# Optimization experiments

Measured on AMD Instinct MI355X. Metric: run time of the kernel, lower is better.

## Reference

```python
import jax, jax.numpy as jnp
import numpy as np

EPS = 1e-5
DIM_HEAD = 64
HEADS = 8

def layernorm(x, gamma, beta):
    mu = jnp.mean(x, axis=-1, keepdims=True)
    var = jnp.var(x, axis=-1, keepdims=True)
    return (x - mu) * jax.lax.rsqrt(var + EPS) * gamma + beta

def setup_inputs() -> dict:
    key = jax.random.key(0)
    ks = jax.random.split(key, 8)
    b, n, dh = 1, 896, 3072       # batch, enformer seq len, enformer_hidden_dim
    c, j, dc = 64, 127, 1024      # num contexts (tracks), context len, context_dim
    inner = HEADS * DIM_HEAD      # 512
    return {
        "embeddings": jax.random.normal(ks[0], (b, n, dh), jnp.float32),
        "context": jax.random.normal(ks[1], (c, j, dc), jnp.float32),
        "context_mask": jax.random.randint(ks[2], (b, j), 0, 2) > 0,
        "q_gamma": jnp.ones((dh,), jnp.float32),
        "q_beta": jnp.zeros((dh,), jnp.float32),
        "kv_gamma": jnp.ones((dc,), jnp.float32),
        "kv_beta": jnp.zeros((dc,), jnp.float32),
        "Wq": jax.random.normal(ks[3], (dh, inner), jnp.float32) * 0.02,
        "Wkv": jax.random.normal(ks[4], (dc, 2 * inner), jnp.float32) * 0.02,
        "null_k": jax.random.normal(ks[5], (inner,), jnp.float32),
        "null_v": jax.random.normal(ks[6], (inner,), jnp.float32),
        "Wo": jax.random.normal(ks[7], (inner, dh), jnp.float32) * 0.02,
        "bo": jnp.zeros((dh,), jnp.float32),
        "Wp": jax.random.normal(jax.random.fold_in(key, 9), (dh, 1), jnp.float32) * 0.02,
        "bp": jnp.zeros((1,), jnp.float32),
    }

def reference(embeddings, context, context_mask, q_gamma, q_beta, kv_gamma, kv_beta,
              Wq, Wkv, null_k, null_v, Wo, bo, Wp, bp):
    h, d = HEADS, DIM_HEAD
    scale = d ** -0.5
    b, n, dh = embeddings.shape
    c = context.shape[0]
    # projections
    q = layernorm(embeddings, q_gamma, q_beta) @ Wq            # (b, n, h*d)
    kv = layernorm(context, kv_gamma, kv_beta) @ Wkv           # (c, j, 2*h*d)
    k, v = jnp.split(kv, 2, axis=-1)
    # prepend null key/value token
    k = jnp.concatenate([jnp.broadcast_to(null_k, (c, 1, h * d)), k], axis=1)
    v = jnp.concatenate([jnp.broadcast_to(null_v, (c, 1, h * d)), v], axis=1)
    # split heads: (b, h, i, d) / (c, h, j, d)
    q = q.reshape(b, n, h, d).transpose(0, 2, 1, 3)
    k = k.reshape(c, -1, h, d).transpose(0, 2, 1, 3)
    v = v.reshape(c, -1, h, d).transpose(0, 2, 1, 3)
    sim = jnp.einsum('bhid,chjd->bchij', q, k) * scale         # (b, c, h, i, j+1)
    # mask: pad with True for the null token, broadcast over c, h, i
    mask = jnp.pad(context_mask, ((0, 0), (1, 0)), constant_values=True)
    sim = jnp.where(mask[:, None, None, None, :], sim, -jnp.finfo(sim.dtype).max)
    attn = jax.nn.softmax(sim, axis=-1)
    out = jnp.einsum('bchij,chjd->bchid', attn, v)             # (b, c, h, i, d)
    out = out.transpose(0, 1, 3, 2, 4).reshape(b, c, n, h * d)  # (b, c, n, h*d)
    branch = out @ Wo + bo                                     # (b, c, n, dh)
    emb = embeddings[:, None] + branch                         # (b, c, n, dh)
    pred = jax.nn.softplus((emb @ Wp + bp)[..., 0])            # (b, c, n)
    return pred.transpose(0, 2, 1)                             # (b, n, c)
```

## Files before the change

kernel.cpp:

```cpp
#include <hip/hip_runtime.h>
#include <math.h>

#define N_SEQ   896
#define DH      3072
#define NCTX    64
#define JLEN    127
#define DC      1024
#define HEADS   8
#define DHEAD   64
#define INNER   512
#define MKV     8128
#define MKVPAD  8192

typedef __bf16 bf16x8 __attribute__((ext_vector_type(8)));
typedef float  f32x4  __attribute__((ext_vector_type(4)));

#define OFF_EDOT   0LL
#define OFF_QBF    (OFF_EDOT + N_SEQ)
#define OFF_KBF    (OFF_QBF  + (long long)N_SEQ*INNER/2)
#define OFF_VPM    (OFF_KBF  + (long long)NCTX*128*INNER/2)
#define OFF_VPNULL (OFF_VPM  + (long long)MKV*8)
#define OFF_WOP    (OFF_VPNULL + 8)
#define OFF_BOP    (OFF_WOP  + INNER)
#define OFF_SBUF   (OFF_BOP  + 16)
#define OFF_ANQ    (OFF_SBUF + (long long)NCTX*HEADS*N_SEQ)
#define OFF_ANKV   (OFF_ANQ  + (long long)N_SEQ*DH/2)
#define OFF_WQT    (OFF_ANKV + (long long)MKVPAD*DC/2)
#define OFF_WKT    (OFF_WQT  + (long long)INNER*DH/2)
#define OFF_WVPT   (OFF_WKT  + (long long)INNER*DC/2)
#define OFF_QSL    (OFF_WVPT + 16*1024/2)

__device__ __forceinline__ void async_copy16(const __bf16* g, __bf16* l) {
    __builtin_amdgcn_global_load_lds(
        (const __attribute__((address_space(1))) unsigned int*)g,
        (__attribute__((address_space(3))) unsigned int*)l,
        16, 0, 0);
}

#define B_Q0   10
#define B_T0   (B_Q0 + 224)
#define B_KV0  (B_T0 + 2048)
#define GRID1  (B_KV0 + 2032)

__global__ __launch_bounds__(256)
void prep_all_kernel(const float* __restrict__ emb, const float* __restrict__ ctx,
                     const float* __restrict__ qg, const float* __restrict__ qb_,
                     const float* __restrict__ kvg, const float* __restrict__ kvb,
                     const float* __restrict__ Wq, const float* __restrict__ Wkv,
                     const float* __restrict__ Wo, const float* __restrict__ bo,
                     const float* __restrict__ Wp,
                     const float* __restrict__ nullk, const float* __restrict__ nullv,
                     __bf16* __restrict__ ANQ, __bf16* __restrict__ ANKV,
                     __bf16* __restrict__ WQT, __bf16* __restrict__ WKT,
                     __bf16* __restrict__ WVPT, float* __restrict__ VPNULL,
                     float* __restrict__ EDOT, float* __restrict__ BOP,
                     __bf16* __restrict__ KBF)
{
    __shared__ float tT[32][33];
    const int bid = blockIdx.x, tid = threadIdx.x;
    const int lane = tid & 63, wid = tid >> 6;

    if (bid < 8) {
        int h = bid;
        float* wops = &tT[0][0];
        int d = tid >> 2, part = tid & 3;
        const float* worow = Wo + (long long)(h * 64 + d) * DH;
        float s = 0.f;
        #pragma unroll 8
        for (int k = part * 4; k < DH; k += 16) {
            float4 a = *(const float4*)&worow[k];
            float4 w = *(const float4*)&Wp[k];
            s += a.x*w.x + a.y*w.y + a.z*w.z + a.w*w.w;
        }
        s += __shfl_xor(s, 1); s += __shfl_xor(s, 2);
        if (part == 0) wops[d] = s;
        __syncthreads();
        if (tid < 64) {
            float v = nullv[h * 64 + tid] * wops[tid];
            #pragma unroll
            for (int o = 1; o < 64; o <<= 1) v += __shfl_xor(v, o);
            if (tid == 0) VPNULL[h] = v;
        }
        #pragma unroll
        for (int kk = 0; kk < 4; ++kk) {
            int k = tid + kk * 256;
            const float* src = Wkv + (long long)k * (2 * INNER) + INNER + h * 64;
            float s2 = 0.f;
            #pragma unroll
            for (int d2 = 0; d2 < 64; d2 += 4) {
                float4 a = *(const float4*)&src[d2];
                s2 += a.x*wops[d2] + a.y*wops[d2+1] + a.z*wops[d2+2] + a.w*wops[d2+3];
            }
            WVPT[h * 1024 + k] = (__bf16)s2;
        }
    } else if (bid == 8) {
        float* red = &tT[0][0];
        float s = 0.f;
        #pragma unroll
        for (int i = 0; i < 3; ++i) {
            int k = i * 1024 + tid * 4;
            float4 a = *(const float4*)&bo[k];
            float4 w = *(const float4*)&Wp[k];
            s += a.x*w.x + a.y*w.y + a.z*w.z + a.w*w.w;
        }
        #pragma unroll
        for (int o = 1; o < 64; o <<= 1) s += __shfl_xor(s, o);
        if (lane == 0) red[wid] = s;
        __syncthreads();
        if (tid == 0) *BOP = red[0] + red[1] + red[2] + red[3];
    } else if (bid == 9) {
        for (int i = tid; i < 8 * 1024; i += 256)
            WVPT[8 * 1024 + i] = (__bf16)0.f;
        for (int i = tid; i < NCTX * INNER; i += 256) {
            int c = i >> 9, d2 = i & 511;
            KBF[(long long)(c * 128) * INNER + d2] = (__bf16)nullk[d2];
        }
    } else if (bid < B_T0) {
        int r = (bid - B_Q0) * 4 + wid;
        const float* x = emb + (long long)r * DH;
        float s = 0.f, ss = 0.f, dp = 0.f;
        #pragma unroll
        for (int c = 0; c < 12; ++c) {
            int col = c * 256 + lane * 4;
            float4 a = *(const float4*)&x[col];
            float4 w = *(const float4*)&Wp[col];
            s  += a.x + a.y + a.z + a.w;
            ss += a.x*a.x + a.y*a.y + a.z*a.z + a.w*a.w;
            dp += a.x*w.x + a.y*w.y + a.z*w.z + a.w*w.w;
        }
        #pragma unroll
        for (int o = 1; o < 64; o <<= 1) {
            s += __shfl_xor(s, o); ss += __shfl_xor(ss, o); dp += __shfl_xor(dp, o);
        }
        float m  = s * (1.f / DH);
        float rs = rsqrtf(ss * (1.f / DH) - m * m + 1e-5f);
        __bf16* op = ANQ + (long long)r * DH;
        #pragma unroll
        for (int c = 0; c < 12; ++c) {
            int col = c * 256 + lane * 4;
            float4 a  = *(const float4*)&x[col];
            float4 g4 = *(const float4*)&qg[col];
            float4 b4 = *(const float4*)&qb_[col];
            __bf16 ov[4];
            ov[0] = (__bf16)((a.x - m) * rs * g4.x + b4.x);
            ov[1] = (__bf16)((a.y - m) * rs * g4.y + b4.y);
            ov[2] = (__bf16)((a.z - m) * rs * g4.z + b4.z);
            ov[3] = (__bf16)((a.w - m) * rs * g4.w + b4.w);
            *(ushort4*)&op[col] = *(ushort4*)ov;
        }
        if (lane == 0) EDOT[r] = dp;
    } else if (bid < B_KV0) {
        int t = bid - B_T0;
        const float* src; __bf16* dst; int srcS, dstS, rb, cb;
        if (t < 1536) {
            rb = (t >> 4) * 32; cb = (t & 15) * 32;
            src = Wq; srcS = INNER; dst = WQT; dstS = DH;
        } else {
            int bi = t - 1536;
            rb = (bi >> 4) * 32; cb = (bi & 15) * 32;
            src = Wkv; srcS = 2 * INNER; dst = WKT; dstS = DC;
        }
        int tx = tid & 31, ty = tid >> 5;
        #pragma unroll
        for (int i = 0; i < 32; i += 8)
            tT[ty + i][tx] = src[(long long)(rb + ty + i) * srcS + cb + tx];
        __syncthreads();
        #pragma unroll
        for (int i = 0; i < 32; i += 8)
            dst[(long long)(cb + ty + i) * dstS + rb + tx] = (__bf16)tT[tx][ty + i];
    } else {
        int r = (bid - B_KV0) * 4 + wid;
        const float* x = ctx + (long long)r * DC;
        float4 xv[4];
        float s = 0.f, ss = 0.f;
        #pragma unroll
        for (int c = 0; c < 4; ++c) {
            xv[c] = *(const float4*)&x[c * 256 + lane * 4];
            s  += xv[c].x + xv[c].y + xv[c].z + xv[c].w;
            ss += xv[c].x*xv[c].x + xv[c].y*xv[c].y + xv[c].z*xv[c].z + xv[c].w*xv[c].w;
        }
        #pragma unroll
        for (int o = 1; o < 64; o <<= 1) { s += __shfl_xor(s, o); ss += __shfl_xor(ss, o); }
        float m  = s * (1.f / DC);
        float rs = rsqrtf(ss * (1.f / DC) - m * m + 1e-5f);
        __bf16* op = ANKV + (long long)r * DC;
        #pragma unroll
        for (int c = 0; c < 4; ++c) {
            int col = c * 256 + lane * 4;
            float4 g4 = *(const float4*)&kvg[col];
            float4 b4 = *(const float4*)&kvb[col];
            __bf16 ov[4];
            ov[0] = (__bf16)((xv[c].x - m) * rs * g4.x + b4.x);
            ov[1] = (__bf16)((xv[c].y - m) * rs * g4.y + b4.y);
            ov[2] = (__bf16)((xv[c].z - m) * rs * g4.z + b4.z);
            ov[3] = (__bf16)((xv[c].w - m) * rs * g4.w + b4.w);
            *(ushort4*)&op[col] = *(ushort4*)ov;
        }
    }
}

__global__ __launch_bounds__(256)
void proj_kernel(const __bf16* __restrict__ ANQ, const __bf16* __restrict__ WQT,
                 const __bf16* __restrict__ ANKV, const __bf16* __restrict__ WKT,
                 const __bf16* __restrict__ WVPT,
                 __bf16* __restrict__ qbf, __bf16* __restrict__ kout,
                 float* __restrict__ vpm) {
    __shared__ __align__(16) __bf16 As[128 * 32];
    __shared__ __align__(16) __bf16 Bs[128 * 32];
    int b = blockIdx.x;
    int tid = threadIdx.x;
    int lane = tid & 63, w = tid >> 6;
    int n16 = lane & 15, quad = lane >> 4;
    int wr = (w >> 1) * 64, wc = (w & 1) * 64;

    const __bf16 *A, *B;
    int K, kend, mode;
    long long m0, n0;
    if (b < 28) {
        mode = 0;
        m0 = (long long)(b % 7) * 128;
        n0 = (long long)(b / 7) * 128;
        K = DH; kend = DH;
        A = ANQ; B = WQT;
    } else {
        mode = 1;
        int b2 = b - 28;
        m0 = (long long)(b2 & 63) * 128;
        n0 = (long long)(b2 >> 6) * 128;
        K = DC; kend = DC;
        A = ANKV; B = WKT;
    }
    bool dovp = (mode == 1) && (n0 == 0);

    const __bf16* aG = A + (m0 + (tid >> 2)) * K + (tid & 3) * 8;
    const __bf16* bG = B + (n0 + (tid >> 2)) * K + (tid & 3) * 8;
    __bf16* aL = As + tid * 8;
    __bf16* bL = Bs + tid * 8;

    f32x4 acc[4][4], accv[4];
    const f32x4 z = {0.f, 0.f, 0.f, 0.f};
    #pragma unroll
    for (int i = 0; i < 4; ++i) {
        accv[i] = z;
        #pragma unroll
        for (int j = 0; j < 4; ++j) acc[i][j] = z;
    }

    for (int k0 = 0; k0 < kend; k0 += 32) {
        async_copy16(aG + k0, aL);
        async_copy16(aG + (long long)64 * K + k0, aL + 2048);
        async_copy16(bG + k0, bL);
        async_copy16(bG + (long long)64 * K + k0, bL + 2048);
        bf16x8 bv;
        if (dovp) bv = *(const bf16x8*)&WVPT[n16 * 1024 + k0 + quad * 8];
        __syncthreads();
        bf16x8 af[4], bfr[4];
        #pragma unroll
        for (int i = 0; i < 4; ++i)
            af[i]  = *(const bf16x8*)&As[(wr + i * 16 + n16) * 32 + quad * 8];
        #pragma unroll
        for (int j = 0; j < 4; ++j)
            bfr[j] = *(const bf16x8*)&Bs[(wc + j * 16 + n16) * 32 + quad * 8];
        #pragma unroll
        for (int i = 0; i < 4; ++i)
            #pragma unroll
            for (int j = 0; j < 4; ++j)
                acc[i][j] = __builtin_amdgcn_mfma_f32_16x16x32_bf16(af[i], bfr[j], acc[i][j], 0, 0, 0);
        if (dovp) {
            #pragma unroll
            for (int i = 0; i < 4; ++i)
                accv[i] = __builtin_amdgcn_mfma_f32_16x16x32_bf16(af[i], bv, accv[i], 0, 0, 0);
        }
        __syncthreads();
    }

    if (mode == 0) {
        #pragma unroll
        for (int i = 0; i < 4; ++i)
            #pragma unroll
            for (int r = 0; r < 4; ++r) {
                long long gr = m0 + wr + i * 16 + quad * 4 + r;
                #pragma unroll
                for (int j = 0; j < 4; ++j) {
                    long long gc = n0 + wc + j * 16 + n16;
                    qbf[gr * INNER + gc] = (__bf16)acc[i][j][r];
                }
            }
    } else {
        #pragma unroll
        for (int i = 0; i < 4; ++i)
            #pragma unroll
            for (int r = 0; r < 4; ++r) {
                long long gr = m0 + wr + i * 16 + quad * 4 + r;
                if (gr >= MKV) continue;
                int cc = (int)(gr / JLEN), jj = (int)(gr % JLEN);
                #pragma unroll
                for (int j = 0; j < 4; ++j) {
                    long long gc = n0 + wc + j * 16 + n16;
                    kout[((long long)(cc * 128) + jj + 1) * INNER + gc] = (__bf16)acc[i][j][r];
                }
                if (dovp && n16 < 8) vpm[gr * 8 + n16] = accv[i][r];
            }
    }
}

#define KROW 72

__global__ __launch_bounds__(256)
void attn_mfma_kernel(const __bf16* __restrict__ qb, const __bf16* __restrict__ kb,
                      const float* __restrict__ vpm, const float* __restrict__ vpnull,
                      const int* __restrict__ mask, float* __restrict__ s_buf) {
    __shared__ __align__(16) __bf16 ksh[128 * KROW];
    __shared__ float vpsh[128];
    __shared__ float amsh[128];
    int ch = blockIdx.y;
    int h = ch & 7, c = ch >> 3;
    int tid = threadIdx.x;
    int lane = tid & 63, w = tid >> 6;
    int n16 = lane & 15, quad = lane >> 4;

    const __bf16* kbase = kb + (long long)(c * 128) * INNER + h * DHEAD;
    #pragma unroll
    for (int p = 0; p < 4; ++p) {
        int chunk = tid + p * 256;
        int row = chunk >> 3, o = chunk & 7;
        bf16x8 v = *(const bf16x8*)(kbase + (long long)row * INNER + o * 8);
        *(bf16x8*)&ksh[row * KROW + o * 8] = v;
    }
    if (tid < 128) {
        vpsh[tid] = (tid == 0) ? vpnull[h] : vpm[(long long)(c * JLEN + tid - 1) * 8 + h];
        amsh[tid] = (tid == 0) ? 0.f : (mask[tid - 1] ? 0.f : -3.0e38f);
    }
    __syncthreads();

    bf16x8 bF[8][2];
    #pragma unroll
    for (int t = 0; t < 8; ++t)
        #pragma unroll
        for (int s = 0; s < 2; ++s)
            bF[t][s] = *(const bf16x8*)&ksh[(t * 16 + n16) * KROW + s * 32 + quad * 8];

    float vpv[8], am[8];
    #pragma unroll
    for (int t = 0; t < 8; ++t) {
        vpv[t] = vpsh[t * 16 + n16];
        am[t]  = amsh[t * 16 + n16];
    }

    const __bf16* qbase = qb + h * DHEAD;
    bf16x8 aF[2][2];
    int r0s[2];
    #pragma unroll
    for (int it2 = 0; it2 < 2; ++it2) {
        int tile = blockIdx.x * 8 + it2 * 4 + w;
        r0s[it2] = tile * 16;
        const __bf16* qrow = qbase + (long long)(r0s[it2] + n16) * INNER + quad * 8;
        aF[it2][0] = *(const bf16x8*)(qrow);
        aF[it2][1] = *(const bf16x8*)(qrow + 32);
    }

    const f32x4 zero = {0.f, 0.f, 0.f, 0.f};
    #pragma unroll
    for (int it2 = 0; it2 < 2; ++it2) {
        int r0 = r0s[it2];
        f32x4 acc[8];
        #pragma unroll
        for (int t = 0; t < 8; ++t) {
            acc[t] = __builtin_amdgcn_mfma_f32_16x16x32_bf16(aF[it2][0], bF[t][0], zero,   0, 0, 0);
            acc[t] = __builtin_amdgcn_mfma_f32_16x16x32_bf16(aF[it2][1], bF[t][1], acc[t], 0, 0, 0);
        }
        float mloc = -3.0e38f;
        #pragma unroll
        for (int t = 0; t < 8; ++t)
            #pragma unroll
            for (int r = 0; r < 4; ++r)
                mloc = fmaxf(mloc, acc[t][r] * 0.125f + am[t]);
        #pragma unroll
        for (int o = 1; o < 16; o <<= 1) mloc = fmaxf(mloc, __shfl_xor(mloc, o, 16));
        float lr[4] = {0.f, 0.f, 0.f, 0.f}, pr[4] = {0.f, 0.f, 0.f, 0.f};
        #pragma unroll
        for (int t = 0; t < 8; ++t) {
            #pragma unroll
            for (int r = 0; r < 4; ++r) {
                float e = __expf(acc[t][r] * 0.125f + am[t] - mloc);
                lr[r] += e; pr[r] += e * vpv[t];
            }
        }
        #pragma unroll
        for (int o = 1; o < 16; o <<= 1) {
            #pragma unroll
            for (int r = 0; r < 4; ++r) {
                lr[r] += __shfl_xor(lr[r], o, 16);
                pr[r] += __shfl_xor(pr[r], o, 16);
            }
        }
        if (n16 == 0) {
            #pragma unroll
            for (int r = 0; r < 4; ++r)
                s_buf[(long long)ch * N_SEQ + r0 + quad * 4 + r] = pr[r] / lr[r];
        }
    }
}

__global__ void final_kernel(const float* __restrict__ s_buf,
                             const float* __restrict__ e_dot,
                             const float* __restrict__ bop,
                             const float* __restrict__ bp,
                             float* __restrict__ out) {
    int t = blockIdx.x * blockDim.x + threadIdx.x;
    if (t >= N_SEQ * NCTX) return;
    int n = t >> 6, c = t & 63;
    float s = 0.f;
    #pragma unroll
    for (int h = 0; h < HEADS; ++h) s += s_buf[((long long)(c * HEADS + h)) * N_SEQ + n];
    float x = e_dot[n] + s + *bop + *bp;
    out[t] = fmaxf(x, 0.f) + log1pf(__expf(-fabsf(x)));
}

extern "C" void kernel_launch(void* const* d_in, const int* in_sizes, int n_in,
                              void* d_out, int out_size, void* d_ws, size_t ws_size,
                              hipStream_t stream) {
    const float* emb   = (const float*)d_in[0];
    const float* ctx   = (const float*)d_in[1];
    const int*   cmask = (const int*)  d_in[2];
    const float* qg    = (const float*)d_in[3];
    const float* qb_   = (const float*)d_in[4];
    const float* kvg   = (const float*)d_in[5];
    const float* kvb   = (const float*)d_in[6];
    const float* Wq    = (const float*)d_in[7];
    const float* Wkv   = (const float*)d_in[8];
    const float* nullk = (const float*)d_in[9];
    const float* nullv = (const float*)d_in[10];
    const float* Wo    = (const float*)d_in[11];
    const float* bo    = (const float*)d_in[12];
    const float* Wp    = (const float*)d_in[13];
    const float* bp    = (const float*)d_in[14];
    float* out  = (float*)d_out;
    float* ws_f = (float*)d_ws;

    float*  EDOT   = ws_f + OFF_EDOT;
    __bf16* QBF    = (__bf16*)(ws_f + OFF_QBF);
    __bf16* KBF    = (__bf16*)(ws_f + OFF_KBF);
    float*  VPM    = ws_f + OFF_VPM;
    float*  VPNULL = ws_f + OFF_VPNULL;
    float*  BOP    = ws_f + OFF_BOP;
    float*  SBUF   = ws_f + OFF_SBUF;
    __bf16* ANQ    = (__bf16*)(ws_f + OFF_ANQ);
    __bf16* ANKV   = (__bf16*)(ws_f + OFF_ANKV);
    __bf16* WQT    = (__bf16*)(ws_f + OFF_WQT);
    __bf16* WKT    = (__bf16*)(ws_f + OFF_WKT);
    __bf16* WVPT   = (__bf16*)(ws_f + OFF_WVPT);

    prep_all_kernel<<<GRID1, 256, 0, stream>>>(
        emb, ctx, qg, qb_, kvg, kvb, Wq, Wkv, Wo, bo, Wp, nullk, nullv,
        ANQ, ANKV, WQT, WKT, WVPT, VPNULL, EDOT, BOP, KBF);
    proj_kernel<<<284, 256, 0, stream>>>(ANQ, WQT, ANKV, WKT, WVPT, QBF, KBF, VPM);
    attn_mfma_kernel<<<dim3(7, NCTX * HEADS), 256, 0, stream>>>(
        QBF, KBF, VPM, VPNULL, cmask, SBUF);
    final_kernel<<<(N_SEQ * NCTX + 255) / 256, 256, 0, stream>>>(SBUF, EDOT, BOP, bp, out);
}
```

Measured before the change: 258.4 us.

## Multi-stage pipeline async global-to-LDS loads in projection GEMM

The projection GEMM's single-buffered load/sync/compute loop is replaced with a software pipeline. Non-VP blocks use a three-stage LDS ring that prefetches two tiles ahead, and VP blocks use double buffering. Explicit vmcnt waits and raw barriers replace __syncthreads so global load latency can overlap with the MFMA work. LDS per block grows threefold, which may reduce occupancy, and the hand-counted vmcnt values must match the actual number of outstanding loads to stay correct.

```diff
diff --git a/kernel.cpp b/kernel.cpp
--- a/kernel.cpp
+++ b/kernel.cpp
@@ -199,14 +199,16 @@
     }
 }
 
+#define STGSZ 4096
+
 __global__ __launch_bounds__(256)
 void proj_kernel(const __bf16* __restrict__ ANQ, const __bf16* __restrict__ WQT,
                  const __bf16* __restrict__ ANKV, const __bf16* __restrict__ WKT,
                  const __bf16* __restrict__ WVPT,
                  __bf16* __restrict__ qbf, __bf16* __restrict__ kout,
                  float* __restrict__ vpm) {
-    __shared__ __align__(16) __bf16 As[128 * 32];
-    __shared__ __align__(16) __bf16 Bs[128 * 32];
+    __shared__ __align__(16) __bf16 As[3 * STGSZ];
+    __shared__ __align__(16) __bf16 Bs[3 * STGSZ];
     int b = blockIdx.x;
     int tid = threadIdx.x;
     int lane = tid & 63, w = tid >> 6;
@@ -234,8 +236,6 @@
 
     const __bf16* aG = A + (m0 + (tid >> 2)) * K + (tid & 3) * 8;
     const __bf16* bG = B + (n0 + (tid >> 2)) * K + (tid & 3) * 8;
-    __bf16* aL = As + tid * 8;
-    __bf16* bL = Bs + tid * 8;
 
     f32x4 acc[4][4], accv[4];
     const f32x4 z = {0.f, 0.f, 0.f, 0.f};
@@ -246,33 +246,86 @@
         for (int j = 0; j < 4; ++j) acc[i][j] = z;
     }
 
-    for (int k0 = 0; k0 < kend; k0 += 32) {
-        async_copy16(aG + k0, aL);
-        async_copy16(aG + (long long)64 * K + k0, aL + 2048);
-        async_copy16(bG + k0, bL);
-        async_copy16(bG + (long long)64 * K + k0, bL + 2048);
+    #define STAGE(stg, k0)                                                      \
+        do {                                                                    \
+            __bf16* aL = As + (stg) * STGSZ + tid * 8;                          \
+            __bf16* bL = Bs + (stg) * STGSZ + tid * 8;                          \
+            async_copy16(aG + (k0), aL);                                        \
+            async_copy16(aG + (long long)64 * K + (k0), aL + 2048);             \
+            async_copy16(bG + (k0), bL);                                        \
+            async_copy16(bG + (long long)64 * K + (k0), bL + 2048);             \
+        } while (0)
+
+    #define FRAGS_MFMA(stg)                                                     \
+        do {                                                                    \
+            const __bf16* cA = As + (stg) * STGSZ;                              \
+            const __bf16* cB = Bs + (stg) * STGSZ;                              \
+            bf16x8 af[4], bfr[4];                                               \
+            _Pragma("unroll")                                                   \
+            for (int i = 0; i < 4; ++i)                                         \
+                af[i]  = *(const bf16x8*)&cA[(wr + i * 16 + n16) * 32 + quad * 8]; \
+            _Pragma("unroll")                                                   \
+            for (int j = 0; j < 4; ++j)                                         \
+                bfr[j] = *(const bf16x8*)&cB[(wc + j * 16 + n16) * 32 + quad * 8]; \
+            _Pragma("unroll")                                                   \
+            for (int i = 0; i < 4; ++i)                                         \
+                _Pragma("unroll")                                               \
+                for (int j = 0; j < 4; ++j)                                     \
+                    acc[i][j] = __builtin_amdgcn_mfma_f32_16x16x32_bf16(af[i], bfr[j], acc[i][j], 0, 0, 0); \
+            if (DOVP_MFMA) {                                                    \
+                _Pragma("unroll")                                               \
+                for (int i = 0; i < 4; ++i)                                     \
+                    accv[i] = __builtin_amdgcn_mfma_f32_16x16x32_bf16(af[i], bv, accv[i], 0, 0, 0); \
+            }                                                                   \
+        } while (0)
+
+    if (!dovp) {
         bf16x8 bv;
-        if (dovp) bv = *(const bf16x8*)&WVPT[n16 * 1024 + k0 + quad * 8];
-        __syncthreads();
-        bf16x8 af[4], bfr[4];
-        #pragma unroll
-        for (int i = 0; i < 4; ++i)
-            af[i]  = *(const bf16x8*)&As[(wr + i * 16 + n16) * 32 + quad * 8];
-        #pragma unroll
-        for (int j = 0; j < 4; ++j)
-            bfr[j] = *(const bf16x8*)&Bs[(wc + j * 16 + n16) * 32 + quad * 8];
-        #pragma unroll
-        for (int i = 0; i < 4; ++i)
-            #pragma unroll
-            for (int j = 0; j < 4; ++j)
-                acc[i][j] = __builtin_amdgcn_mfma_f32_16x16x32_bf16(af[i], bfr[j], acc[i][j], 0, 0, 0);
-        if (dovp) {
-            #pragma unroll
-            for (int i = 0; i < 4; ++i)
-                accv[i] = __builtin_amdgcn_mfma_f32_16x16x32_bf16(af[i], bv, accv[i], 0, 0, 0);
-        }
-        __syncthreads();
-    }
+        #define DOVP_MFMA 0
+        STAGE(0, 0);
+        STAGE(1, 32);
+        int cur = 0;
+        for (int k0 = 0; k0 < kend; k0 += 32) {
+            int kpre = k0 + 64;
+            if (kpre < kend) {
+                int pre = cur + 2; if (pre >= 3) pre -= 3;
+                STAGE(pre, kpre);
+                asm volatile("s_waitcnt vmcnt(8)" ::: "memory");
+            } else if (k0 + 32 < kend) {
+                asm volatile("s_waitcnt vmcnt(4)" ::: "memory");
+            } else {
+                asm volatile("s_waitcnt vmcnt(0)" ::: "memory");
+            }
+            __builtin_amdgcn_s_barrier();
+            FRAGS_MFMA(cur);
+            __builtin_amdgcn_s_barrier();
+            ++cur; if (cur >= 3) cur -= 3;
+        }
+        #undef DOVP_MFMA
+    } else {
+        #define DOVP_MFMA 1
+        STAGE(0, 0);
+        bf16x8 bv  = *(const bf16x8*)&WVPT[n16 * 1024 + 0 + quad * 8];
+        int cur = 0;
+        for (int k0 = 0; k0 < kend; k0 += 32) {
+            bf16x8 bvn;
+            if (k0 + 32 < kend) {
+                bvn = *(const bf16x8*)&WVPT[n16 * 1024 + (k0 + 32) + quad * 8];
+                STAGE(cur ^ 1, k0 + 32);
+                asm volatile("s_waitcnt vmcnt(5)" ::: "memory");
+            } else {
+                asm volatile("s_waitcnt vmcnt(0)" ::: "memory");
+            }
+            __builtin_amdgcn_s_barrier();
+            FRAGS_MFMA(cur);
+            __builtin_amdgcn_s_barrier();
+            bv = bvn;
+            cur ^= 1;
+        }
+        #undef DOVP_MFMA
+    }
+    #undef STAGE
+    #undef FRAGS_MFMA
 
     if (mode == 0) {
         #pragma unroll
```

New measurement: 254.5 us. About the same (-1.5%).

## Split-K the Q projection GEMM across eight slices with atomic fp32 accumulation

Applied to the files above, without the earlier changes.

The Q projection (896x512, K=3072) previously ran on only 28 blocks, each looping over the full K dimension, which made it the long tail of proj_kernel. It is now split into 8 K-slices of 384, giving 224 blocks that atomically add into a zeroed fp32 buffer. Extra prep blocks zero that buffer, and the attention kernel reads fp32 Q and converts it to bf16. In exchange this adds global atomics, zeroing traffic, doubled Q read bytes, and a non-deterministic summation order.

```diff
diff --git a/kernel.cpp b/kernel.cpp
--- a/kernel.cpp
+++ b/kernel.cpp
@@ -28,7 +28,7 @@
 #define OFF_WQT    (OFF_ANKV + (long long)MKVPAD*DC/2)
 #define OFF_WKT    (OFF_WQT  + (long long)INNER*DH/2)
 #define OFF_WVPT   (OFF_WKT  + (long long)INNER*DC/2)
-#define OFF_QSL    (OFF_WVPT + 16*1024/2)
+#define OFF_QS     (OFF_WVPT + 16*1024/2)
 
 __device__ __forceinline__ void async_copy16(const __bf16* g, __bf16* l) {
     __builtin_amdgcn_global_load_lds(
@@ -37,7 +37,9 @@
         16, 0, 0);
 }
 
-#define B_Q0   10
+#define B_Z0   10
+#define NZB    112
+#define B_Q0   (B_Z0 + NZB)
 #define B_T0   (B_Q0 + 224)
 #define B_KV0  (B_T0 + 2048)
 #define GRID1  (B_KV0 + 2032)
@@ -54,7 +56,7 @@
                      __bf16* __restrict__ WQT, __bf16* __restrict__ WKT,
                      __bf16* __restrict__ WVPT, float* __restrict__ VPNULL,
                      float* __restrict__ EDOT, float* __restrict__ BOP,
-                     __bf16* __restrict__ KBF)
+                     __bf16* __restrict__ KBF, float* __restrict__ QS)
 {
     __shared__ float tT[32][33];
     const int bid = blockIdx.x, tid = threadIdx.x;
@@ -115,6 +117,12 @@
             int c = i >> 9, d2 = i & 511;
             KBF[(long long)(c * 128) * INNER + d2] = (__bf16)nullk[d2];
         }
+    } else if (bid < B_Q0) {
+        float4* q4 = (float4*)QS;
+        const float4 z4 = {0.f, 0.f, 0.f, 0.f};
+        int base = (bid - B_Z0) * 1024;
+        #pragma unroll
+        for (int k = 0; k < 4; ++k) q4[base + k * 256 + tid] = z4;
     } else if (bid < B_T0) {
         int r = (bid - B_Q0) * 4 + wid;
         const float* x = emb + (long long)r * DH;
@@ -203,7 +211,7 @@
 void proj_kernel(const __bf16* __restrict__ ANQ, const __bf16* __restrict__ WQT,
                  const __bf16* __restrict__ ANKV, const __bf16* __restrict__ WKT,
                  const __bf16* __restrict__ WVPT,
-                 __bf16* __restrict__ qbf, __bf16* __restrict__ kout,
+                 float* __restrict__ qs, __bf16* __restrict__ kout,
                  float* __restrict__ vpm) {
     __shared__ __align__(16) __bf16 As[128 * 32];
     __shared__ __align__(16) __bf16 Bs[128 * 32];
@@ -214,20 +222,22 @@
     int wr = (w >> 1) * 64, wc = (w & 1) * 64;
 
     const __bf16 *A, *B;
-    int K, kend, mode;
+    int K, kbeg, kend, mode;
     long long m0, n0;
-    if (b < 28) {
+    if (b < 224) {
         mode = 0;
-        m0 = (long long)(b % 7) * 128;
-        n0 = (long long)(b / 7) * 128;
-        K = DH; kend = DH;
+        int slice = b / 28;
+        int rem = b % 28;
+        m0 = (long long)(rem % 7) * 128;
+        n0 = (long long)(rem / 7) * 128;
+        K = DH; kbeg = slice * 384; kend = kbeg + 384;
         A = ANQ; B = WQT;
     } else {
         mode = 1;
-        int b2 = b - 28;
+        int b2 = b - 224;
         m0 = (long long)(b2 & 63) * 128;
         n0 = (long long)(b2 >> 6) * 128;
-        K = DC; kend = DC;
+        K = DC; kbeg = 0; kend = DC;
         A = ANKV; B = WKT;
     }
     bool dovp = (mode == 1) && (n0 == 0);
@@ -246,7 +256,7 @@
         for (int j = 0; j < 4; ++j) acc[i][j] = z;
     }
 
-    for (int k0 = 0; k0 < kend; k0 += 32) {
+    for (int k0 = kbeg; k0 < kend; k0 += 32) {
         async_copy16(aG + k0, aL);
         async_copy16(aG + (long long)64 * K + k0, aL + 2048);
         async_copy16(bG + k0, bL);
@@ -283,7 +293,7 @@
                 #pragma unroll
                 for (int j = 0; j < 4; ++j) {
                     long long gc = n0 + wc + j * 16 + n16;
-                    qbf[gr * INNER + gc] = (__bf16)acc[i][j][r];
+                    atomicAdd(&qs[gr * INNER + gc], acc[i][j][r]);
                 }
             }
     } else {
@@ -307,7 +317,7 @@
 #define KROW 72
 
 __global__ __launch_bounds__(256)
-void attn_mfma_kernel(const __bf16* __restrict__ qb, const __bf16* __restrict__ kb,
+void attn_mfma_kernel(const float* __restrict__ qs, const __bf16* __restrict__ kb,
                       const float* __restrict__ vpm, const float* __restrict__ vpnull,
                       const int* __restrict__ mask, float* __restrict__ s_buf) {
     __shared__ __align__(16) __bf16 ksh[128 * KROW];
@@ -347,16 +357,24 @@
         am[t]  = amsh[t * 16 + n16];
     }
 
-    const __bf16* qbase = qb + h * DHEAD;
     bf16x8 aF[2][2];
     int r0s[2];
     #pragma unroll
     for (int it2 = 0; it2 < 2; ++it2) {
         int tile = blockIdx.x * 8 + it2 * 4 + w;
         r0s[it2] = tile * 16;
-        const __bf16* qrow = qbase + (long long)(r0s[it2] + n16) * INNER + quad * 8;
-        aF[it2][0] = *(const bf16x8*)(qrow);
-        aF[it2][1] = *(const bf16x8*)(qrow + 32);
+        const float* qrow = qs + (long long)(r0s[it2] + n16) * INNER + h * DHEAD + quad * 8;
+        float4 a0 = *(const float4*)(qrow);
+        float4 a1 = *(const float4*)(qrow + 4);
+        float4 b0 = *(const float4*)(qrow + 32);
+        float4 b1 = *(const float4*)(qrow + 36);
+        bf16x8 v0, v1;
+        v0[0] = (__bf16)a0.x; v0[1] = (__bf16)a0.y; v0[2] = (__bf16)a0.z; v0[3] = (__bf16)a0.w;
+        v0[4] = (__bf16)a1.x; v0[5] = (__bf16)a1.y; v0[6] = (__bf16)a1.z; v0[7] = (__bf16)a1.w;
+        v1[0] = (__bf16)b0.x; v1[1] = (__bf16)b0.y; v1[2] = (__bf16)b0.z; v1[3] = (__bf16)b0.w;
+        v1[4] = (__bf16)b1.x; v1[5] = (__bf16)b1.y; v1[6] = (__bf16)b1.z; v1[7] = (__bf16)b1.w;
+        aF[it2][0] = v0;
+        aF[it2][1] = v1;
     }
 
     const f32x4 zero = {0.f, 0.f, 0.f, 0.f};
@@ -439,7 +457,6 @@
     float* ws_f = (float*)d_ws;
 
     float*  EDOT   = ws_f + OFF_EDOT;
-    __bf16* QBF    = (__bf16*)(ws_f + OFF_QBF);
     __bf16* KBF    = (__bf16*)(ws_f + OFF_KBF);
     float*  VPM    = ws_f + OFF_VPM;
     float*  VPNULL = ws_f + OFF_VPNULL;
@@ -450,12 +467,13 @@
     __bf16* WQT    = (__bf16*)(ws_f + OFF_WQT);
     __bf16* WKT    = (__bf16*)(ws_f + OFF_WKT);
     __bf16* WVPT   = (__bf16*)(ws_f + OFF_WVPT);
+    float*  QS     = ws_f + OFF_QS;
 
     prep_all_kernel<<<GRID1, 256, 0, stream>>>(
         emb, ctx, qg, qb_, kvg, kvb, Wq, Wkv, Wo, bo, Wp, nullk, nullv,
-        ANQ, ANKV, WQT, WKT, WVPT, VPNULL, EDOT, BOP, KBF);
-    proj_kernel<<<284, 256, 0, stream>>>(ANQ, WQT, ANKV, WKT, WVPT, QBF, KBF, VPM);
+        ANQ, ANKV, WQT, WKT, WVPT, VPNULL, EDOT, BOP, KBF, QS);
+    proj_kernel<<<480, 256, 0, stream>>>(ANQ, WQT, ANKV, WKT, WVPT, QS, KBF, VPM);
     attn_mfma_kernel<<<dim3(7, NCTX * HEADS), 256, 0, stream>>>(
-        QBF, KBF, VPM, VPNULL, cmask, SBUF);
+        QS, KBF, VPM, VPNULL, cmask, SBUF);
     final_kernel<<<(N_SEQ * NCTX + 255) / 256, 256, 0, stream>>>(SBUF, EDOT, BOP, bp, out);
 }
```

After: 235.4 us. 8.9% less time.
